# Kernel tuning notes

Measured on AMD Instinct MI355X. Metric: run time of the kernel, lower is better.

Reference implementation:

```python
import jax, jax.numpy as jnp
import numpy as np

B, N, DIM = 4, 2048, 1024
H, DH = 16, 64
SCALE = DH ** -0.5


def setup_inputs() -> dict:
    key = jax.random.key(0)
    k1, k2, k3, k4 = jax.random.split(key, 4)
    x = jax.random.normal(k1, (B, N, DIM), dtype=jnp.float32)
    mask = jax.random.randint(k2, (B, N, N), 0, 2, dtype=jnp.int32)
    W_qkv = jax.random.normal(k3, (DIM, 3 * H * DH), dtype=jnp.float32) * (DIM ** -0.5)
    W_out = jax.random.normal(k4, (H * DH, DIM), dtype=jnp.float32) * ((H * DH) ** -0.5)
    b_out = jnp.zeros((DIM,), dtype=jnp.float32)
    return {"x": x, "mask": mask, "W_qkv": W_qkv, "W_out": W_out, "b_out": b_out}


def reference(x, mask, W_qkv, W_out, b_out):
    # QKV projection: [b, n, 3*h*d]
    qkv = x @ W_qkv
    q, k, v = jnp.split(qkv, 3, axis=-1)
    # 'b n (h d) -> b h n d'
    def to_heads(t):
        b, n, _ = t.shape
        return t.reshape(b, n, H, DH).transpose(0, 2, 1, 3)
    q, k, v = to_heads(q), to_heads(k), to_heads(v)
    # scaled dot-product scores: [b, h, n, n]
    scores = jnp.einsum('bhnd,bhmd->bhnm', q, k) * SCALE
    scores = jnp.where(mask[:, None, :, :] == 1, -jnp.inf, scores)
    att = jax.nn.softmax(scores, axis=-1)
    out = jnp.einsum('bhnm,bhmd->bhnd', att, v)
    # 'b h n d -> b n (h d)'
    out = out.transpose(0, 2, 1, 3).reshape(x.shape[0], x.shape[1], H * DH)
    return out @ W_out + b_out
```

## Files before the change

kernel.cpp:

```cpp
#include <hip/hip_runtime.h>
#include <hip/hip_bf16.h>


typedef __attribute__((ext_vector_type(8))) short bf16x8;
typedef __attribute__((ext_vector_type(4))) float f32x4;

__device__ __forceinline__ unsigned short f2bf(float f) {
  unsigned u = __builtin_bit_cast(unsigned, f);
  u += 0x7fffu + ((u >> 16) & 1u);
  return (unsigned short)(u >> 16);
}

__device__ __forceinline__ void gload16(const void* g, void* l) {
  __builtin_amdgcn_global_load_lds(
      (const __attribute__((address_space(1))) unsigned int*)g,
      (__attribute__((address_space(3))) unsigned int*)l, 16, 0, 0);
}

__device__ __forceinline__ bf16x8 ldsw(const short* base, int row, int elem) {
  const char* p = (const char*)base + row * 128 + ((elem * 2) ^ ((row & 7) << 4));
  return *(const bf16x8*)p;
}

__global__ __launch_bounds__(256) void k_cvt(const float* __restrict__ in,
                                             unsigned short* __restrict__ out) {
  int i = (blockIdx.x * 256 + threadIdx.x) * 4;
  float4 v = *reinterpret_cast<const float4*>(in + i);
  ushort4 o;
  o.x = f2bf(v.x); o.y = f2bf(v.y); o.z = f2bf(v.z); o.w = f2bf(v.w);
  *reinterpret_cast<ushort4*>(out + i) = o;
}

__global__ __launch_bounds__(256) void k_transpose_cvt(const float* __restrict__ in,
                                                       unsigned short* __restrict__ out,
                                                       int rows, int cols) {
  __shared__ float tile[32][33];
  int tx = threadIdx.x & 31, ty = threadIdx.x >> 5;
  int c0 = blockIdx.x * 32, r0 = blockIdx.y * 32;
#pragma unroll
  for (int i = 0; i < 32; i += 8)
    tile[ty + i][tx] = in[(size_t)(r0 + ty + i) * cols + (c0 + tx)];
  __syncthreads();
#pragma unroll
  for (int i = 0; i < 32; i += 8)
    out[(size_t)(c0 + ty + i) * rows + (r0 + tx)] = f2bf(tile[tx][ty + i]);
}

__global__ __launch_bounds__(256) void k_packmask(const int* __restrict__ mask,
                                                  unsigned long long* __restrict__ pack) {
  const int row = blockIdx.x;
  const int t = threadIdx.x, w = t >> 6, lane = t & 63;
  const int* mrow = mask + (size_t)row * 2048;
#pragma unroll
  for (int it = 0; it < 8; ++it) {
    int key = it * 256 + w * 64 + lane;
    unsigned long long bal = __ballot(mrow[key] == 1);
    if (lane == 0) pack[(size_t)row * 32 + it * 4 + w] = bal;
  }
}

template <int EPI>
__global__ __launch_bounds__(256) void k_gemm(
    const unsigned short* __restrict__ A, const unsigned short* __restrict__ Bt,
    unsigned short* __restrict__ Qo, unsigned short* __restrict__ Ko,
    unsigned short* __restrict__ Vo, float* __restrict__ Co,
    const float* __restrict__ bias) {
  __shared__ __align__(16) short As[128 * 64];
  __shared__ __align__(16) short Bs[128 * 64];
  const int t = threadIdx.x;
  const int bn = blockIdx.x, bm = blockIdx.y;
  const int wid = t >> 6, lane = t & 63, g = lane >> 4, l15 = lane & 15;
  const int wr = wid >> 1, wc = wid & 1;
  f32x4 zero = {0.f, 0.f, 0.f, 0.f};
  f32x4 acc[4][4];
#pragma unroll
  for (int i = 0; i < 4; ++i)
#pragma unroll
    for (int j = 0; j < 4; ++j) acc[i][j] = zero;

  const char* Ab = (const char*)(A + (size_t)bm * 128 * 1024);
  const char* Bb = (const char*)(Bt + (size_t)bn * 128 * 1024);

  for (int k0 = 0; k0 < 2048; k0 += 128) {
#pragma unroll
    for (int q = 0; q < 4; ++q) {
      int idx = t + q * 256, r = idx >> 3, c = idx & 7;
      int sw = (c * 16) ^ ((r & 7) << 4);
      gload16(Ab + (size_t)r * 2048 + k0 + sw, (char*)As + idx * 16);
      gload16(Bb + (size_t)r * 2048 + k0 + sw, (char*)Bs + idx * 16);
    }
    asm volatile("s_waitcnt vmcnt(0)" ::: "memory");
    __syncthreads();
#pragma unroll
    for (int ks = 0; ks < 2; ++ks) {
      bf16x8 a[4], b[4];
#pragma unroll
      for (int mi = 0; mi < 4; ++mi) a[mi] = ldsw(As, wr * 64 + mi * 16 + l15, ks * 32 + g * 8);
#pragma unroll
      for (int ni = 0; ni < 4; ++ni) b[ni] = ldsw(Bs, wc * 64 + ni * 16 + l15, ks * 32 + g * 8);
#pragma unroll
      for (int mi = 0; mi < 4; ++mi)
#pragma unroll
        for (int ni = 0; ni < 4; ++ni)
          acc[mi][ni] = __builtin_amdgcn_mfma_f32_16x16x32_bf16(a[mi], b[ni], acc[mi][ni], 0, 0, 0);
    }
    __syncthreads();
  }

#pragma unroll
  for (int mi = 0; mi < 4; ++mi) {
#pragma unroll
    for (int ni = 0; ni < 4; ++ni) {
#pragma unroll
      for (int j = 0; j < 4; ++j) {
        float v = acc[mi][ni][j];
        int row = bm * 128 + wr * 64 + mi * 16 + g * 4 + j;
        int col = bn * 128 + wc * 64 + ni * 16 + l15;
        if (EPI == 0) {
          int b = row >> 11, nn = row & 2047;
          int s = col >> 10, rem = col & 1023;
          int h = rem >> 6, d = rem & 63;
          int bh = b * 16 + h;
          if (s == 0) Qo[(((size_t)bh) * 2048 + nn) * 64 + d] = f2bf(v * 0.18033688011112042f);
          else if (s == 1) Ko[(((size_t)bh) * 2048 + nn) * 64 + d] = f2bf(v);
          else Vo[(((size_t)bh) * 64 + d) * 2048 + nn] = f2bf(v);
        } else {
          Co[(size_t)row * 1024 + col] = v + bias[col];
        }
      }
    }
  }
}

__global__ __launch_bounds__(512, 8) void k_attn(
    const unsigned short* __restrict__ Q, const unsigned short* __restrict__ K,
    const unsigned short* __restrict__ Vt_g, const unsigned long long* __restrict__ pack,
    unsigned short* __restrict__ O) {
  __shared__ __align__(16) short Ks[2][64 * 64];
  __shared__ __align__(16) short Vt[2][64 * 64];
  __shared__ __align__(16) short Ps[8][16 * 32];
  const int bid0 = blockIdx.x;
  const int bid = (bid0 & 7) * 128 + (bid0 >> 3);
  const int qt = bid & 15, bh = bid >> 4;
  const int b = bh >> 4;
  const int t = threadIdx.x, wid = t >> 6, lane = t & 63, g = lane >> 4, l15 = lane & 15;
  const char* Kb = (const char*)(K + (size_t)bh * (2048 * 64));
  const char* Vb = (const char*)(Vt_g + (size_t)bh * (64 * 2048));
  const unsigned short* Qb = Q + (size_t)bh * (2048 * 64);

  const int sr = t >> 3, sc = t & 7;
  const int sw_src = (sc * 16) ^ ((sr & 7) << 4);
  char* PwB = (char*)&Ps[wid][0];
  const int ps_rd  = (l15 * 64 + g * 16) ^ ((l15 & 7) << 4);
  const int ps_wr0 = (l15 * 64 + g * 8) ^ ((l15 & 7) << 4);

  gload16(Kb + (size_t)sr * 128 + sw_src, (char*)&Ks[0][0] + t * 16);
  gload16(Vb + (size_t)sr * 4096 + sw_src, (char*)&Vt[0][0] + t * 16);
  const int qrow = qt * 128 + wid * 16 + l15;
  bf16x8 qf0 = *reinterpret_cast<const bf16x8*>(Qb + (size_t)qrow * 64 + g * 8);
  bf16x8 qf1 = *reinterpret_cast<const bf16x8*>(Qb + (size_t)qrow * 64 + 32 + g * 8);
  const unsigned long long* mrow = pack + ((size_t)b * 2048 + qrow) * 32;
  asm volatile("s_waitcnt vmcnt(0)" ::: "memory");
  __syncthreads();

  f32x4 zero = {0.f, 0.f, 0.f, 0.f};
  f32x4 oacc[4];
#pragma unroll
  for (int nf = 0; nf < 4; ++nf) oacc[nf] = zero;
  float lp = 0.f;

  int cb = 0;
#pragma unroll 1
  for (int kt = 0; kt < 32; ++kt) {
    const int nb = cb ^ 1;
    unsigned long long mw = mrow[kt];
    if (kt + 1 < 32) {
      gload16(Kb + (size_t)((kt + 1) * 64 + sr) * 128 + sw_src, (char*)&Ks[nb][0] + t * 16);
      gload16(Vb + (size_t)sr * 4096 + (kt + 1) * 128 + sw_src, (char*)&Vt[nb][0] + t * 16);
    }
    unsigned mlo = (unsigned)mw >> (g * 4);
    unsigned mhi = (unsigned)(mw >> 32) >> (g * 4);
#pragma unroll
    for (int kh = 0; kh < 2; ++kh) {
      f32x4 sf[2] = {zero, zero};
      __builtin_amdgcn_s_setprio(1);
#pragma unroll
      for (int ds = 0; ds < 2; ++ds) {
        bf16x8 qk = ds ? qf1 : qf0;
#pragma unroll
        for (int nf2 = 0; nf2 < 2; ++nf2) {
          bf16x8 kk = ldsw(&Ks[cb][0], (kh * 2 + nf2) * 16 + l15, ds * 32 + g * 8);
          sf[nf2] = __builtin_amdgcn_mfma_f32_16x16x32_bf16(kk, qk, sf[nf2], 0, 0, 0);
        }
      }
      __builtin_amdgcn_s_setprio(0);
      unsigned msrc = kh ? mhi : mlo;
#pragma unroll
      for (int nf2 = 0; nf2 < 2; ++nf2) {
        unsigned eu[4];
#pragma unroll
        for (int j = 0; j < 4; ++j) {
          float s = sf[nf2][j];
          if (msrc & (1u << (nf2 * 16 + j))) s = -1e30f;
          float e = __builtin_amdgcn_exp2f(s);
          lp += e;
          eu[j] = __builtin_bit_cast(unsigned, e);
        }
        uint2 pk;
        pk.x = __builtin_amdgcn_perm(eu[1], eu[0], 0x07060302);
        pk.y = __builtin_amdgcn_perm(eu[3], eu[2], 0x07060302);
        *reinterpret_cast<uint2*>(PwB + (nf2 ? (ps_wr0 ^ 32) : ps_wr0)) = pk;
      }
      asm volatile("s_waitcnt lgkmcnt(0)" ::: "memory");
      __builtin_amdgcn_sched_barrier(0);
      bf16x8 ap = *reinterpret_cast<const bf16x8*>(PwB + ps_rd);
      __builtin_amdgcn_s_setprio(1);
#pragma unroll
      for (int nf = 0; nf < 4; ++nf) {
        bf16x8 bv = ldsw(&Vt[cb][0], nf * 16 + l15, kh * 32 + g * 8);
        oacc[nf] = __builtin_amdgcn_mfma_f32_16x16x32_bf16(ap, bv, oacc[nf], 0, 0, 0);
      }
      __builtin_amdgcn_s_setprio(0);
    }
    asm volatile("s_waitcnt vmcnt(0)" ::: "memory");
    __syncthreads();
    cb = nb;
  }

  float l = lp;
  l += __shfl_xor(l, 16);
  l += __shfl_xor(l, 32);
  float invl = 1.0f / l;
  float inv[4];
#pragma unroll
  for (int j = 0; j < 4; ++j) inv[j] = __shfl(invl, g * 4 + j);

  const int h = bh & 15;
#pragma unroll
  for (int nf = 0; nf < 4; ++nf) {
#pragma unroll
    for (int j = 0; j < 4; ++j) {
      int qg = qt * 128 + wid * 16 + g * 4 + j;
      int d = nf * 16 + l15;
      O[((size_t)b * 2048 + qg) * 1024 + h * 64 + d] = f2bf(oacc[nf][j] * inv[j]);
    }
  }
}

extern "C" void kernel_launch(void* const* d_in, const int* in_sizes, int n_in,
                              void* d_out, int out_size, void* d_ws, size_t ws_size,
                              hipStream_t stream) {
  (void)in_sizes; (void)n_in; (void)out_size; (void)ws_size;
  const float* x = (const float*)d_in[0];
  const int* mask = (const int*)d_in[1];
  const float* Wqkv = (const float*)d_in[2];
  const float* Wout = (const float*)d_in[3];
  const float* bout = (const float*)d_in[4];
  float* out = (float*)d_out;

  unsigned short* ws = (unsigned short*)d_ws;
  unsigned short* Xb   = ws;
  unsigned short* Wq_t = Xb + 8388608;
  unsigned short* Wo_t = Wq_t + 3145728;
  unsigned short* Qa   = Wo_t + 1048576;
  unsigned short* Ka   = Qa + 8388608;
  unsigned short* Va   = Ka + 8388608;
  unsigned short* ATT  = Va + 8388608;
  unsigned long long* MP = (unsigned long long*)(ATT + 8388608);

  k_cvt<<<8192, 256, 0, stream>>>(x, Xb);
  k_transpose_cvt<<<dim3(96, 32), 256, 0, stream>>>(Wqkv, Wq_t, 1024, 3072);
  k_transpose_cvt<<<dim3(32, 32), 256, 0, stream>>>(Wout, Wo_t, 1024, 1024);
  k_packmask<<<8192, 256, 0, stream>>>(mask, MP);
  k_gemm<0><<<dim3(24, 64), 256, 0, stream>>>(Xb, Wq_t, Qa, Ka, Va, nullptr, nullptr);
  k_attn<<<1024, 512, 0, stream>>>(Qa, Ka, Va, MP, ATT);
  k_gemm<1><<<dim3(8, 64), 256, 0, stream>>>(ATT, Wo_t, nullptr, nullptr, nullptr, out, bout);
}
```

Before: 252.8 us.

## Stage QKV epilogue through LDS for coalesced stores; compute row sums via MFMA

The QKV GEMM epilogue now writes bf16 tiles into shared memory, padded to 132 elements per row and transposed for V, then emits 16-byte coalesced global stores instead of scattered 2-byte stores. The attention kernel drops the per-element scalar accumulation of softmax denominators. Instead it adds one extra MFMA per sub-tile that multiplies P by a ones column, so the row sums come out of the matrix unit. This removes VALU adds but adds MFMA work, and the sums are now taken from bf16-rounded probabilities rather than fp32 values.

Measured after the change: 257.5 us. Within noise of the previous version (+1.8%).

```diff
diff --git a/kernel.cpp b/kernel.cpp
--- a/kernel.cpp
+++ b/kernel.cpp
@@ -65,8 +65,9 @@
     unsigned short* __restrict__ Qo, unsigned short* __restrict__ Ko,
     unsigned short* __restrict__ Vo, float* __restrict__ Co,
     const float* __restrict__ bias) {
-  __shared__ __align__(16) short As[128 * 64];
-  __shared__ __align__(16) short Bs[128 * 64];
+  __shared__ __align__(16) short Smem[16896];
+  short* As = Smem;
+  short* Bs = Smem + 8192;
   const int t = threadIdx.x;
   const int bn = blockIdx.x, bm = blockIdx.y;
   const int wid = t >> 6, lane = t & 63, g = lane >> 4, l15 = lane & 15;
@@ -107,27 +108,70 @@
     __syncthreads();
   }
 
-#pragma unroll
-  for (int mi = 0; mi < 4; ++mi) {
-#pragma unroll
-    for (int ni = 0; ni < 4; ++ni) {
-#pragma unroll
-      for (int j = 0; j < 4; ++j) {
-        float v = acc[mi][ni][j];
-        int row = bm * 128 + wr * 64 + mi * 16 + g * 4 + j;
-        int col = bn * 128 + wc * 64 + ni * 16 + l15;
-        if (EPI == 0) {
-          int b = row >> 11, nn = row & 2047;
-          int s = col >> 10, rem = col & 1023;
-          int h = rem >> 6, d = rem & 63;
-          int bh = b * 16 + h;
-          if (s == 0) Qo[(((size_t)bh) * 2048 + nn) * 64 + d] = f2bf(v * 0.18033688011112042f);
-          else if (s == 1) Ko[(((size_t)bh) * 2048 + nn) * 64 + d] = f2bf(v);
-          else Vo[(((size_t)bh) * 64 + d) * 2048 + nn] = f2bf(v);
-        } else {
-          Co[(size_t)row * 1024 + col] = v + bias[col];
+  if (EPI == 1) {
+#pragma unroll
+    for (int mi = 0; mi < 4; ++mi)
+#pragma unroll
+      for (int ni = 0; ni < 4; ++ni)
+#pragma unroll
+        for (int j = 0; j < 4; ++j) {
+          int row = bm * 128 + wr * 64 + mi * 16 + g * 4 + j;
+          int col = bn * 128 + wc * 64 + ni * 16 + l15;
+          Co[(size_t)row * 1024 + col] = acc[mi][ni][j] + bias[col];
         }
+    return;
+  }
+
+  const int s = bn >> 3;
+  const int h0 = (bn & 7) * 2;
+  const int bglob = (bm * 128) >> 11;
+  const int n0 = (bm * 128) & 2047;
+
+  if (s < 2) {
+    const float qs = (s == 0) ? 0.18033688011112042f : 1.0f;
+#pragma unroll
+    for (int mi = 0; mi < 4; ++mi)
+#pragma unroll
+      for (int ni = 0; ni < 4; ++ni)
+#pragma unroll
+        for (int j = 0; j < 4; ++j)
+          Smem[(wr * 64 + mi * 16 + g * 4 + j) * 132 + wc * 64 + ni * 16 + l15] =
+              (short)f2bf(acc[mi][ni][j] * qs);
+    __syncthreads();
+    int r = t >> 1, hh = t & 1;
+    unsigned short* dst = (s == 0 ? Qo : Ko) +
+        (((size_t)(bglob * 16 + h0 + hh)) * 2048 + n0 + r) * 64;
+    const short* src = Smem + r * 132 + hh * 64;
+#pragma unroll
+    for (int k = 0; k < 8; ++k) {
+      uint2 a = *reinterpret_cast<const uint2*>(src + k * 8);
+      uint2 b2 = *reinterpret_cast<const uint2*>(src + k * 8 + 4);
+      uint4 w = {a.x, a.y, b2.x, b2.y};
+      *reinterpret_cast<uint4*>(dst + k * 8) = w;
+    }
+  } else {
+#pragma unroll
+    for (int mi = 0; mi < 4; ++mi)
+#pragma unroll
+      for (int ni = 0; ni < 4; ++ni) {
+        unsigned x0 = f2bf(acc[mi][ni][0]), x1 = f2bf(acc[mi][ni][1]);
+        unsigned x2 = f2bf(acc[mi][ni][2]), x3 = f2bf(acc[mi][ni][3]);
+        uint2 pk = {x0 | (x1 << 16), x2 | (x3 << 16)};
+        int col = wc * 64 + ni * 16 + l15;
+        int row = wr * 64 + mi * 16 + g * 4;
+        *reinterpret_cast<uint2*>(Smem + col * 132 + row) = pk;
       }
+    __syncthreads();
+    int c = t >> 1, seg = t & 1;
+    int h = h0 + (c >> 6), d = c & 63;
+    unsigned short* dst = Vo + ((size_t)(bglob * 16 + h) * 64 + d) * 2048 + n0 + seg * 64;
+    const short* src = Smem + c * 132 + seg * 64;
+#pragma unroll
+    for (int k = 0; k < 8; ++k) {
+      uint2 a = *reinterpret_cast<const uint2*>(src + k * 8);
+      uint2 b2 = *reinterpret_cast<const uint2*>(src + k * 8 + 4);
+      uint4 w = {a.x, a.y, b2.x, b2.y};
+      *reinterpret_cast<uint4*>(dst + k * 8) = w;
     }
   }
 }
@@ -154,6 +198,13 @@
   const int ps_rd  = (l15 * 64 + g * 16) ^ ((l15 & 7) << 4);
   const int ps_wr0 = (l15 * 64 + g * 8) ^ ((l15 & 7) << 4);
 
+  bf16x8 onesf;
+  {
+    short ov = (l15 == 0) ? (short)0x3F80 : (short)0;
+#pragma unroll
+    for (int i = 0; i < 8; ++i) onesf[i] = ov;
+  }
+
   gload16(Kb + (size_t)sr * 128 + sw_src, (char*)&Ks[0][0] + t * 16);
   gload16(Vb + (size_t)sr * 4096 + sw_src, (char*)&Vt[0][0] + t * 16);
   const int qrow = qt * 128 + wid * 16 + l15;
@@ -167,7 +218,7 @@
   f32x4 oacc[4];
 #pragma unroll
   for (int nf = 0; nf < 4; ++nf) oacc[nf] = zero;
-  float lp = 0.f;
+  f32x4 sumacc = zero;
 
   int cb = 0;
 #pragma unroll 1
@@ -203,7 +254,6 @@
           float s = sf[nf2][j];
           if (msrc & (1u << (nf2 * 16 + j))) s = -1e30f;
           float e = __builtin_amdgcn_exp2f(s);
-          lp += e;
           eu[j] = __builtin_bit_cast(unsigned, e);
         }
         uint2 pk;
@@ -220,6 +270,7 @@
         bf16x8 bv = ldsw(&Vt[cb][0], nf * 16 + l15, kh * 32 + g * 8);
         oacc[nf] = __builtin_amdgcn_mfma_f32_16x16x32_bf16(ap, bv, oacc[nf], 0, 0, 0);
       }
+      sumacc = __builtin_amdgcn_mfma_f32_16x16x32_bf16(ap, onesf, sumacc, 0, 0, 0);
       __builtin_amdgcn_s_setprio(0);
     }
     asm volatile("s_waitcnt vmcnt(0)" ::: "memory");
@@ -227,13 +278,12 @@
     cb = nb;
   }
 
-  float l = lp;
-  l += __shfl_xor(l, 16);
-  l += __shfl_xor(l, 32);
-  float invl = 1.0f / l;
   float inv[4];
 #pragma unroll
-  for (int j = 0; j < 4; ++j) inv[j] = __shfl(invl, g * 4 + j);
+  for (int j = 0; j < 4; ++j) {
+    float sj = __shfl(sumacc[j], lane & 48);
+    inv[j] = 1.0f / sj;
+  }
 
   const int h = bh & 15;
 #pragma unroll
```
